# Kernel optimization log

Measured on AMD Instinct MI355X. Metric: run time of the kernel, lower is better.

## Reference

```python
import jax, jax.numpy as jnp
import numpy as np

B, T, C, H = 8, 2048, 1024, 128  # batch, seq (== block_size), embed dim, head size


def setup_inputs() -> dict:
    key = jax.random.key(0)
    kx, kq, kk, kv = jax.random.split(key, 4)
    x = jax.random.normal(kx, (B, T, C), dtype=jnp.float32)
    # torch Linear(no bias) weights: [head_size, in_features], applied as x @ W.T
    s = 1.0 / np.sqrt(C)
    Wq = jax.random.normal(kq, (H, C), dtype=jnp.float32) * s
    Wk = jax.random.normal(kk, (H, C), dtype=jnp.float32) * s
    Wv = jax.random.normal(kv, (H, C), dtype=jnp.float32) * s
    return {"x": x, "Wq": Wq, "Wk": Wk, "Wv": Wv}


def reference(x, Wq, Wk, Wv):
    # projections: [B,T,C] @ [C,H] -> [B,T,H]
    q = jnp.einsum('btc,hc->bth', x, Wq)
    k = jnp.einsum('btc,hc->bth', x, Wk)
    v = jnp.einsum('btc,hc->bth', x, Wv)
    scale = k.shape[-1] ** -0.5
    # scores [B,T,T], causal mask, softmax in fp32 (autocast disabled in original)
    scores = jnp.einsum('bqh,bkh->bqk', q, k) * scale
    causal = jnp.tril(jnp.ones((T, T), dtype=bool))
    scores = jnp.where(causal, scores, -jnp.inf)
    attn = jax.nn.softmax(scores.astype(jnp.float32), axis=-1)
    # dropout_rate = 0.0 -> identity
    out = jnp.einsum('bqk,bkh->bqh', attn.astype(v.dtype), v)
    return out
```

## Files before the change

kernel.cpp:

```cpp
#include <hip/hip_runtime.h>
#include <hip/hip_bf16.h>

constexpr int NB = 8;
constexpr int T  = 2048;
constexpr int C  = 1024;
constexpr int Hd = 128;

typedef short bf16x8 __attribute__((ext_vector_type(8)));
typedef float floatx4 __attribute__((ext_vector_type(4)));

__device__ __forceinline__ ushort f2bf(float x) {
    return __builtin_bit_cast(ushort, __float2bfloat16(x));
}
__device__ __forceinline__ float bf2f(ushort u) {
    unsigned int x = ((unsigned int)u) << 16;
    return __builtin_bit_cast(float, x);
}
__device__ __forceinline__ void async16(ushort* lds, const ushort* g) {
    __builtin_amdgcn_global_load_lds(
        (const __attribute__((address_space(1))) unsigned int*)g,
        (__attribute__((address_space(3))) unsigned int*)lds, 16, 0, 0);
}

__global__ __launch_bounds__(256) void convert_xw(
    const float* __restrict__ X, const float* __restrict__ Wq,
    const float* __restrict__ Wk, const float* __restrict__ Wv,
    ushort* __restrict__ Xb, ushort* __restrict__ Wb)
{
    int bid = blockIdx.x;
    if (bid < 8192) {
        size_t i = ((size_t)bid * 256 + threadIdx.x) * 8;
        float4 a = *(const float4*)&X[i];
        float4 b = *(const float4*)&X[i + 4];
        bf16x8 o;
        o[0] = (short)f2bf(a.x); o[1] = (short)f2bf(a.y);
        o[2] = (short)f2bf(a.z); o[3] = (short)f2bf(a.w);
        o[4] = (short)f2bf(b.x); o[5] = (short)f2bf(b.y);
        o[6] = (short)f2bf(b.z); o[7] = (short)f2bf(b.w);
        *(bf16x8*)&Xb[i] = o;
    } else {
        int g = (bid - 8192) * 256 + threadIdx.x;
        size_t base = (size_t)g * 8;
        int sel = (int)(base >> 17);
        const float* W = sel == 0 ? Wq : (sel == 1 ? Wk : Wv);
        float s = (sel == 0) ? 0.12751744f : 1.0f;
        size_t off = base - (size_t)sel * 131072;
        float4 a = *(const float4*)&W[off];
        float4 b = *(const float4*)&W[off + 4];
        bf16x8 o;
        o[0] = (short)f2bf(a.x * s); o[1] = (short)f2bf(a.y * s);
        o[2] = (short)f2bf(a.z * s); o[3] = (short)f2bf(a.w * s);
        o[4] = (short)f2bf(b.x * s); o[5] = (short)f2bf(b.y * s);
        o[6] = (short)f2bf(b.z * s); o[7] = (short)f2bf(b.w * s);
        *(bf16x8*)&Wb[base] = o;
    }
}

__global__ __launch_bounds__(256) void qkv_gemm(
    const ushort* __restrict__ Xb, const ushort* __restrict__ Wb,
    ushort* __restrict__ Qo, ushort* __restrict__ Ko, ushort* __restrict__ Vt)
{
    __shared__ ushort SM[24576];
    ushort* Al = SM;
    ushort* Bl = SM + 16384;
    const int m0 = blockIdx.x * 128;
    const int n0 = blockIdx.y * 64;
    const int tid = threadIdx.x, lane = tid & 63, wave = tid >> 6;
    const int quad = lane >> 4, colL = lane & 15;
    const int wm = (wave & 1) * 64, wn = (wave >> 1) * 32;
    const int lr4 = lane >> 4;
    const int cg  = lane & 15;

    floatx4 acc[4][2] = {};

    for (int k0 = 0; k0 < C; k0 += 128) {
        for (int t = 0; t < 8; ++t) {
            int q = wave * 8 + t;
            int row = q * 4 + lr4;
            async16(&Al[q * 512 + lane * 8],
                    &Xb[(size_t)(m0 + row) * C + k0 + ((cg ^ (row & 7)) * 8)]);
        }
        for (int t = 0; t < 4; ++t) {
            int q = wave * 4 + t;
            int row = q * 4 + lr4;
            async16(&Bl[q * 512 + lane * 8],
                    &Wb[(size_t)(n0 + row) * C + k0 + ((cg ^ (row & 7)) * 8)]);
        }
        __syncthreads();

        for (int kk = 0; kk < 4; ++kk) {
            bf16x8 af[4], bfr[2];
            for (int mt = 0; mt < 4; ++mt)
                af[mt] = *(const bf16x8*)
                    &Al[(wm + mt * 16 + colL) * 128 + (((kk * 4 + quad) ^ (colL & 7))) * 8];
            for (int nt = 0; nt < 2; ++nt)
                bfr[nt] = *(const bf16x8*)
                    &Bl[(wn + nt * 16 + colL) * 128 + (((kk * 4 + quad) ^ (colL & 7))) * 8];
            for (int mt = 0; mt < 4; ++mt)
                for (int nt = 0; nt < 2; ++nt)
                    acc[mt][nt] = __builtin_amdgcn_mfma_f32_16x16x32_bf16(
                        af[mt], bfr[nt], acc[mt][nt], 0, 0, 0);
        }
        __syncthreads();
    }

    const int sel = n0 >> 7;
    const int h0 = n0 & 127;
    if (sel < 2) {
        ushort* dst = sel == 0 ? Qo : Ko;
        for (int mt = 0; mt < 4; ++mt)
            for (int nt = 0; nt < 2; ++nt)
                for (int r = 0; r < 4; ++r) {
                    int row = m0 + wm + mt * 16 + quad * 4 + r;
                    int h = h0 + wn + nt * 16 + colL;
                    dst[(size_t)row * Hd + h] = f2bf(acc[mt][nt][r]);
                }
    } else {
        ushort* TL = SM;
        for (int mt = 0; mt < 4; ++mt)
            for (int nt = 0; nt < 2; ++nt)
                for (int r = 0; r < 4; ++r)
                    TL[(wm + mt * 16 + quad * 4 + r) * 66 + wn + nt * 16 + colL] =
                        f2bf(acc[mt][nt][r]);
        __syncthreads();
        const int b = m0 >> 11, tb = m0 & 2047;
        const int h = tid & 63, tq = tid >> 6;
        for (int st = 0; st < 4; ++st) {
            int t0 = tq * 32 + st * 8;
            bf16x8 o;
            for (int jx = 0; jx < 8; ++jx)
                o[jx] = (short)TL[(t0 + jx) * 66 + h];
            *(bf16x8*)&Vt[((size_t)b * Hd + h0 + h) * T + tb + t0] = o;
        }
    }
}

__global__ __launch_bounds__(256, 2) void attn_flash(
    const ushort* __restrict__ Q, const ushort* __restrict__ Kg,
    const ushort* __restrict__ Vt, float* __restrict__ out)
{
    __shared__ ushort Kl[2][128 * 128];
    __shared__ ushort Vl[2][128 * 128];
    __shared__ ushort Pl[4][16 * 128];

    const int tid = threadIdx.x, lane = tid & 63, wave = tid >> 6;
    const int quad = lane >> 4, colL = lane & 15;

    const int id = blockIdx.x;
    const int b = id & 7;
    const int qt = 31 - (id >> 3);
    const int q0 = qt * 64;
    const int cmax = (q0 + 63) >> 7;

    const int r16 = tid >> 4, p16 = tid & 15;

    {
        for (int t = 0; t < 8; ++t) {
            int row = t * 16 + r16;
            async16(&Kl[0][t * 2048 + tid * 8],
                    &Kg[((size_t)b * T + row) * Hd + ((p16 ^ (row & 15)) * 8)]);
        }
        for (int t = 0; t < 8; ++t) {
            int hrow = t * 16 + r16;
            async16(&Vl[0][t * 2048 + tid * 8],
                    &Vt[((size_t)b * Hd + hrow) * T + ((p16 ^ (hrow & 15)) * 8)]);
        }
    }
    bf16x8 qa[4];
    {
        const ushort* qp =
            &Q[((size_t)b * T + q0 + wave * 16 + colL) * Hd + quad * 8];
        for (int ks = 0; ks < 4; ++ks)
            qa[ks] = *(const bf16x8*)&qp[ks * 32];
    }

    floatx4 Oacc[8] = {};
    float l_p[4] = {0.f, 0.f, 0.f, 0.f};

    ushort* Pw = &Pl[wave][0];

    for (int c = 0; c <= cmax; ++c) {
        const int cur = c & 1;
        __syncthreads();

        if (c < cmax) {
            const int k0 = (c + 1) * 128;
            const int nxt = cur ^ 1;
            for (int t = 0; t < 8; ++t) {
                int row = t * 16 + r16;
                async16(&Kl[nxt][t * 2048 + tid * 8],
                        &Kg[((size_t)b * T + k0 + row) * Hd + ((p16 ^ (row & 15)) * 8)]);
            }
            for (int t = 0; t < 8; ++t) {
                int hrow = t * 16 + r16;
                async16(&Vl[nxt][t * 2048 + tid * 8],
                        &Vt[((size_t)b * Hd + hrow) * T + k0 + ((p16 ^ (hrow & 15)) * 8)]);
            }
        }

        floatx4 accS[8] = {};
        for (int ks = 0; ks < 4; ++ks)
            for (int nt = 0; nt < 8; ++nt) {
                int krow = nt * 16 + colL;
                bf16x8 kb = *(const bf16x8*)
                    &Kl[cur][krow * 128 + (((ks * 4 + quad) ^ colL) * 8)];
                accS[nt] = __builtin_amdgcn_mfma_f32_16x16x32_bf16(qa[ks], kb, accS[nt], 0, 0, 0);
            }

        if (c == cmax) {
            const int k0 = c * 128;
            for (int nt = 0; nt < 8; ++nt)
                for (int rr = 0; rr < 4; ++rr) {
                    int lrow = q0 + wave * 16 + quad * 4 + rr;
                    int lcol = k0 + nt * 16 + colL;
                    if (lcol > lrow) accS[nt][rr] = -__builtin_inff();
                }
        }

        for (int nt = 0; nt < 8; ++nt)
            for (int rr = 0; rr < 4; ++rr) {
                float p = __builtin_amdgcn_exp2f(fminf(accS[nt][rr], 14.f));
                l_p[rr] += p;
                int prow = quad * 4 + rr;
                Pw[prow * 128 + ((nt * 16 + colL) ^ ((prow & 7) << 4))] = f2bf(p);
            }

        bf16x8 pa[4];
        {
            const int prow = colL;
            const int sw = (prow & 7) << 4;
            for (int ks = 0; ks < 4; ++ks)
                pa[ks] = *(const bf16x8*)&Pw[prow * 128 + ((ks * 32 + quad * 8) ^ sw)];
        }

        for (int ks = 0; ks < 4; ++ks)
            for (int th = 0; th < 8; ++th) {
                int hrow = th * 16 + colL;
                bf16x8 vb = *(const bf16x8*)
                    &Vl[cur][hrow * 128 + (((ks * 4 + quad) ^ colL) * 8)];
                Oacc[th] = __builtin_amdgcn_mfma_f32_16x16x32_bf16(pa[ks], vb, Oacc[th], 0, 0, 0);
            }
    }

    float inv[4];
    for (int rr = 0; rr < 4; ++rr) {
        float s = l_p[rr];
        for (int off = 1; off < 16; off <<= 1)
            s += __shfl_xor(s, off, 64);
        inv[rr] = 1.0f / s;
    }
    for (int th = 0; th < 8; ++th)
        for (int rr = 0; rr < 4; ++rr) {
            int row = q0 + wave * 16 + quad * 4 + rr;
            out[((size_t)b * T + row) * Hd + th * 16 + colL] = Oacc[th][rr] * inv[rr];
        }
}

extern "C" void kernel_launch(void* const* d_in, const int* in_sizes, int n_in,
                              void* d_out, int out_size, void* d_ws, size_t ws_size,
                              hipStream_t stream) {
    const float* x  = (const float*)d_in[0];
    const float* Wq = (const float*)d_in[1];
    const float* Wk = (const float*)d_in[2];
    const float* Wv = (const float*)d_in[3];
    float* out = (float*)d_out;

    char* w = (char*)d_ws;
    ushort* Xb = (ushort*)w;  w += (size_t)33554432;
    ushort* Wb = (ushort*)w;  w += (size_t)786432;
    ushort* Qb  = (ushort*)w;  w += (size_t)NB * T * Hd * 2;
    ushort* Kb  = (ushort*)w;  w += (size_t)NB * T * Hd * 2;
    ushort* Vtb = (ushort*)w;  w += (size_t)NB * T * Hd * 2;

    convert_xw<<<8384, 256, 0, stream>>>(x, Wq, Wk, Wv, Xb, Wb);
    qkv_gemm<<<dim3(128, 6), 256, 0, stream>>>(Xb, Wb, Qb, Kb, Vtb);
    attn_flash<<<256, 256, 0, stream>>>(Qb, Kb, Vtb, out);
}
```

Baseline: 160.9 us.

## Split attention KV range across two blocks and combine partial outputs

Splits each query tile's key/value chunks between two blocks using interleaved even and odd chunks. Each block writes unnormalized bf16 partial outputs and row sums, and a new combine kernel adds them and normalizes. This doubles the grid from 256 to 512 blocks so the GPU is filled better. To cut LDS it also drops double buffering, reusing the K buffer for P and reloading K and V within the loop with extra barriers. The cost is an extra kernel launch, a round trip of partials through memory, and less overlap of loads with compute.

```diff
diff --git a/kernel.cpp b/kernel.cpp
--- a/kernel.cpp
+++ b/kernel.cpp
@@ -135,37 +135,27 @@
     }
 }
 
-__global__ __launch_bounds__(256, 2) void attn_flash(
+__global__ __launch_bounds__(256, 2) void attn_partial(
     const ushort* __restrict__ Q, const ushort* __restrict__ Kg,
-    const ushort* __restrict__ Vt, float* __restrict__ out)
+    const ushort* __restrict__ Vt, ushort* __restrict__ Opart,
+    float* __restrict__ lpart)
 {
-    __shared__ ushort Kl[2][128 * 128];
-    __shared__ ushort Vl[2][128 * 128];
-    __shared__ ushort Pl[4][16 * 128];
+    __shared__ ushort Kl[128 * 128];
+    __shared__ ushort Vl[128 * 128];
 
     const int tid = threadIdx.x, lane = tid & 63, wave = tid >> 6;
     const int quad = lane >> 4, colL = lane & 15;
 
     const int id = blockIdx.x;
-    const int b = id & 7;
-    const int qt = 31 - (id >> 3);
+    const int s  = id & 1;
+    const int bq = id >> 1;
+    const int b  = bq & 7;
+    const int qt = 31 - (bq >> 3);
     const int q0 = qt * 64;
     const int cmax = (q0 + 63) >> 7;
 
     const int r16 = tid >> 4, p16 = tid & 15;
 
-    {
-        for (int t = 0; t < 8; ++t) {
-            int row = t * 16 + r16;
-            async16(&Kl[0][t * 2048 + tid * 8],
-                    &Kg[((size_t)b * T + row) * Hd + ((p16 ^ (row & 15)) * 8)]);
-        }
-        for (int t = 0; t < 8; ++t) {
-            int hrow = t * 16 + r16;
-            async16(&Vl[0][t * 2048 + tid * 8],
-                    &Vt[((size_t)b * Hd + hrow) * T + ((p16 ^ (hrow & 15)) * 8)]);
-        }
-    }
     bf16x8 qa[4];
     {
         const ushort* qp =
@@ -177,83 +167,145 @@
     floatx4 Oacc[8] = {};
     float l_p[4] = {0.f, 0.f, 0.f, 0.f};
 
-    ushort* Pw = &Pl[wave][0];
-
-    for (int c = 0; c <= cmax; ++c) {
-        const int cur = c & 1;
-        __syncthreads();
-
-        if (c < cmax) {
-            const int k0 = (c + 1) * 128;
-            const int nxt = cur ^ 1;
+    if (s <= cmax) {
+        {
+            const int k0 = s * 128;
             for (int t = 0; t < 8; ++t) {
                 int row = t * 16 + r16;
-                async16(&Kl[nxt][t * 2048 + tid * 8],
+                async16(&Kl[t * 2048 + tid * 8],
                         &Kg[((size_t)b * T + k0 + row) * Hd + ((p16 ^ (row & 15)) * 8)]);
             }
             for (int t = 0; t < 8; ++t) {
                 int hrow = t * 16 + r16;
-                async16(&Vl[nxt][t * 2048 + tid * 8],
+                async16(&Vl[t * 2048 + tid * 8],
                         &Vt[((size_t)b * Hd + hrow) * T + k0 + ((p16 ^ (hrow & 15)) * 8)]);
             }
         }
 
-        floatx4 accS[8] = {};
-        for (int ks = 0; ks < 4; ++ks)
-            for (int nt = 0; nt < 8; ++nt) {
-                int krow = nt * 16 + colL;
-                bf16x8 kb = *(const bf16x8*)
-                    &Kl[cur][krow * 128 + (((ks * 4 + quad) ^ colL) * 8)];
-                accS[nt] = __builtin_amdgcn_mfma_f32_16x16x32_bf16(qa[ks], kb, accS[nt], 0, 0, 0);
-            }
-
-        if (c == cmax) {
-            const int k0 = c * 128;
+        for (int c = s; c <= cmax; c += 2) {
+            __syncthreads();
+
+            floatx4 accS[8] = {};
+            for (int ks = 0; ks < 4; ++ks)
+                for (int nt = 0; nt < 8; ++nt) {
+                    int krow = nt * 16 + colL;
+                    bf16x8 kb = *(const bf16x8*)
+                        &Kl[krow * 128 + (((ks * 4 + quad) ^ colL) * 8)];
+                    accS[nt] = __builtin_amdgcn_mfma_f32_16x16x32_bf16(qa[ks], kb, accS[nt], 0, 0, 0);
+                }
+
+            if (c == cmax) {
+                const int k0 = c * 128;
+                for (int nt = 0; nt < 8; ++nt)
+                    for (int rr = 0; rr < 4; ++rr) {
+                        int lrow = q0 + wave * 16 + quad * 4 + rr;
+                        int lcol = k0 + nt * 16 + colL;
+                        if (lcol > lrow) accS[nt][rr] = -__builtin_inff();
+                    }
+            }
+            __syncthreads();
+
+            ushort* Pw = &Kl[wave * 2048];
             for (int nt = 0; nt < 8; ++nt)
                 for (int rr = 0; rr < 4; ++rr) {
-                    int lrow = q0 + wave * 16 + quad * 4 + rr;
-                    int lcol = k0 + nt * 16 + colL;
-                    if (lcol > lrow) accS[nt][rr] = -__builtin_inff();
-                }
-        }
-
-        for (int nt = 0; nt < 8; ++nt)
-            for (int rr = 0; rr < 4; ++rr) {
-                float p = __builtin_amdgcn_exp2f(fminf(accS[nt][rr], 14.f));
-                l_p[rr] += p;
-                int prow = quad * 4 + rr;
-                Pw[prow * 128 + ((nt * 16 + colL) ^ ((prow & 7) << 4))] = f2bf(p);
-            }
-
-        bf16x8 pa[4];
-        {
-            const int prow = colL;
-            const int sw = (prow & 7) << 4;
+                    float p = __builtin_amdgcn_exp2f(fminf(accS[nt][rr], 14.f));
+                    l_p[rr] += p;
+                    int prow = quad * 4 + rr;
+                    Pw[prow * 128 + ((nt * 16 + colL) ^ ((prow & 7) << 4))] = f2bf(p);
+                }
+
+            bf16x8 pa[4];
+            {
+                const int prow = colL;
+                const int sw = (prow & 7) << 4;
+                for (int ks = 0; ks < 4; ++ks)
+                    pa[ks] = *(const bf16x8*)&Pw[prow * 128 + ((ks * 32 + quad * 8) ^ sw)];
+            }
+            __syncthreads();
+
+            if (c + 2 <= cmax) {
+                const int k0 = (c + 2) * 128;
+                for (int t = 0; t < 8; ++t) {
+                    int row = t * 16 + r16;
+                    async16(&Kl[t * 2048 + tid * 8],
+                            &Kg[((size_t)b * T + k0 + row) * Hd + ((p16 ^ (row & 15)) * 8)]);
+                }
+            }
+
             for (int ks = 0; ks < 4; ++ks)
-                pa[ks] = *(const bf16x8*)&Pw[prow * 128 + ((ks * 32 + quad * 8) ^ sw)];
-        }
-
-        for (int ks = 0; ks < 4; ++ks)
-            for (int th = 0; th < 8; ++th) {
-                int hrow = th * 16 + colL;
-                bf16x8 vb = *(const bf16x8*)
-                    &Vl[cur][hrow * 128 + (((ks * 4 + quad) ^ colL) * 8)];
-                Oacc[th] = __builtin_amdgcn_mfma_f32_16x16x32_bf16(pa[ks], vb, Oacc[th], 0, 0, 0);
-            }
-    }
-
-    float inv[4];
+                for (int th = 0; th < 8; ++th) {
+                    int hrow = th * 16 + colL;
+                    bf16x8 vb = *(const bf16x8*)
+                        &Vl[hrow * 128 + (((ks * 4 + quad) ^ colL) * 8)];
+                    Oacc[th] = __builtin_amdgcn_mfma_f32_16x16x32_bf16(pa[ks], vb, Oacc[th], 0, 0, 0);
+                }
+
+            if (c + 2 <= cmax) {
+                __syncthreads();
+                const int k0 = (c + 2) * 128;
+                for (int t = 0; t < 8; ++t) {
+                    int hrow = t * 16 + r16;
+                    async16(&Vl[t * 2048 + tid * 8],
+                            &Vt[((size_t)b * Hd + hrow) * T + k0 + ((p16 ^ (hrow & 15)) * 8)]);
+                }
+            }
+        }
+    }
+
+    float l_r[4];
     for (int rr = 0; rr < 4; ++rr) {
-        float s = l_p[rr];
+        float v = l_p[rr];
         for (int off = 1; off < 16; off <<= 1)
-            s += __shfl_xor(s, off, 64);
-        inv[rr] = 1.0f / s;
-    }
+            v += __shfl_xor(v, off, 64);
+        l_r[rr] = v;
+    }
+    ushort* Op = &Opart[(size_t)id * 8192];
     for (int th = 0; th < 8; ++th)
         for (int rr = 0; rr < 4; ++rr) {
-            int row = q0 + wave * 16 + quad * 4 + rr;
-            out[((size_t)b * T + row) * Hd + th * 16 + colL] = Oacc[th][rr] * inv[rr];
-        }
+            int row = wave * 16 + quad * 4 + rr;
+            Op[row * 128 + th * 16 + colL] = f2bf(Oacc[th][rr]);
+        }
+    if (colL == 0)
+        for (int rr = 0; rr < 4; ++rr) {
+            int row = wave * 16 + quad * 4 + rr;
+            lpart[(size_t)id * 64 + row] = l_r[rr];
+        }
+}
+
+__global__ __launch_bounds__(256) void attn_combine(
+    const ushort* __restrict__ Opart, const float* __restrict__ lpart,
+    float* __restrict__ out)
+{
+    const int bq = blockIdx.x;
+    const int b  = bq & 7;
+    const int qt = 31 - (bq >> 3);
+    const int t = threadIdx.x;
+    const int row_l = t >> 2;
+    const int c32 = (t & 3) * 32;
+
+    const float l = lpart[(size_t)(bq * 2) * 64 + row_l] +
+                    lpart[(size_t)(bq * 2 + 1) * 64 + row_l];
+    const float inv = 1.0f / l;
+
+    const ushort* p0 = &Opart[(size_t)(bq * 2) * 8192 + row_l * 128 + c32];
+    const ushort* p1 = &Opart[(size_t)(bq * 2 + 1) * 8192 + row_l * 128 + c32];
+    float* dst = &out[((size_t)b * T + qt * 64 + row_l) * Hd + c32];
+
+    for (int x = 0; x < 4; ++x) {
+        bf16x8 a = *(const bf16x8*)&p0[x * 8];
+        bf16x8 bb = *(const bf16x8*)&p1[x * 8];
+        float4 o0, o1;
+        o0.x = (bf2f((ushort)a[0]) + bf2f((ushort)bb[0])) * inv;
+        o0.y = (bf2f((ushort)a[1]) + bf2f((ushort)bb[1])) * inv;
+        o0.z = (bf2f((ushort)a[2]) + bf2f((ushort)bb[2])) * inv;
+        o0.w = (bf2f((ushort)a[3]) + bf2f((ushort)bb[3])) * inv;
+        o1.x = (bf2f((ushort)a[4]) + bf2f((ushort)bb[4])) * inv;
+        o1.y = (bf2f((ushort)a[5]) + bf2f((ushort)bb[5])) * inv;
+        o1.z = (bf2f((ushort)a[6]) + bf2f((ushort)bb[6])) * inv;
+        o1.w = (bf2f((ushort)a[7]) + bf2f((ushort)bb[7])) * inv;
+        *(float4*)&dst[x * 8] = o0;
+        *(float4*)&dst[x * 8 + 4] = o1;
+    }
 }
 
 extern "C" void kernel_launch(void* const* d_in, const int* in_sizes, int n_in,
@@ -266,7 +318,10 @@
     float* out = (float*)d_out;
 
     char* w = (char*)d_ws;
-    ushort* Xb = (ushort*)w;  w += (size_t)33554432;
+    ushort* Xb = (ushort*)w;
+    ushort* Opart = (ushort*)w;
+    float* lpart  = (float*)(w + (size_t)512 * 8192 * 2);
+    w += (size_t)33554432;
     ushort* Wb = (ushort*)w;  w += (size_t)786432;
     ushort* Qb  = (ushort*)w;  w += (size_t)NB * T * Hd * 2;
     ushort* Kb  = (ushort*)w;  w += (size_t)NB * T * Hd * 2;
@@ -274,5 +329,6 @@
 
     convert_xw<<<8384, 256, 0, stream>>>(x, Wq, Wk, Wv, Xb, Wb);
     qkv_gemm<<<dim3(128, 6), 256, 0, stream>>>(Xb, Wb, Qb, Kb, Vtb);
-    attn_flash<<<256, 256, 0, stream>>>(Qb, Kb, Vtb, out);
-}
+    attn_partial<<<512, 256, 0, stream>>>(Qb, Kb, Vtb, Opart, lpart);
+    attn_combine<<<256, 256, 0, stream>>>(Opart, lpart, out);
+}
```

New measurement: 152.3 us. -5.3%, faster.
